# Kernel tuning notes

Hardware: AMD Instinct MI355X
Metric: run time of the kernel (lower is better)

The kernel has to match this reference:

```python
import jax, jax.numpy as jnp
import numpy as np

EMBED_DIM = 1024
NUM_HEADS = 16
HEAD_DIM = EMBED_DIM // NUM_HEADS


def setup_inputs() -> dict:
    key = jax.random.key(0)
    ks = jax.random.split(key, 5)
    B, N, E = 2, 2048, EMBED_DIM
    scale = E ** -0.5
    return {
        "x": jax.random.normal(ks[0], (B, N, E), dtype=jnp.float32),
        "w_qkv": jax.random.normal(ks[1], (E, 3 * E), dtype=jnp.float32) * scale,
        "b_qkv": jnp.zeros((3 * E,), dtype=jnp.float32),
        "w_proj": jax.random.normal(ks[2], (E, E), dtype=jnp.float32) * scale,
        "b_proj": jnp.zeros((E,), dtype=jnp.float32),
    }


def reference(x, w_qkv, b_qkv, w_proj, b_proj):
    B, N, E = x.shape
    H, D = NUM_HEADS, HEAD_DIM
    qkv = x @ w_qkv + b_qkv                      # [B,N,3E]
    qkv = qkv.reshape(B, N, 3, H, D)
    q = qkv[:, :, 0].transpose(0, 2, 1, 3)        # [B,H,N,D]
    k = qkv[:, :, 1].transpose(0, 2, 1, 3)
    v = qkv[:, :, 2].transpose(0, 2, 1, 3)
    attn = jnp.einsum('bhnd,bhmd->bhnm', q, k) * (D ** -0.5)
    attn = jax.nn.softmax(attn, axis=-1)          # dropout is identity in eval mode
    out = jnp.einsum('bhnm,bhmd->bhnd', attn, v)  # [B,H,N,D]
    out = out.transpose(0, 2, 1, 3).reshape(B, N, E)
    return out @ w_proj + b_proj
```

## Files before the change

kernel.cpp:

```cpp
#include <hip/hip_runtime.h>
#include <hip/hip_bf16.h>
#include <cstdint>
#include <cstddef>


typedef __attribute__((ext_vector_type(8))) short short8;
typedef __attribute__((ext_vector_type(4))) short short4v;
typedef __attribute__((ext_vector_type(4))) float f32x4;

#define MFMA16(a, b, c) __builtin_amdgcn_mfma_f32_16x16x32_bf16((a), (b), (c), 0, 0, 0)
#define EXP2F(x) __builtin_amdgcn_exp2f(x)

__device__ __forceinline__ float b2f(short s) {
  union { unsigned u; float f; } x; x.u = ((unsigned)(unsigned short)s) << 16; return x.f;
}
__device__ __forceinline__ short f2b(float f) {
  union { __hip_bfloat16 h; short s; } u; u.h = __float2bfloat16(f); return u.s;
}
__device__ __forceinline__ void async_lds16(const void* g, void* l) {
  __builtin_amdgcn_global_load_lds(
      (const __attribute__((address_space(1))) void*)g,
      (__attribute__((address_space(3))) void*)l, 16, 0, 0);
}

__global__ __launch_bounds__(256) void cast_f32_bf16(const float* __restrict__ in,
                                                     short* __restrict__ out, int n4) {
  for (int idx = blockIdx.x * 256 + threadIdx.x; idx < n4; idx += 1024 * 256) {
    f32x4 v = ((const f32x4*)in)[idx];
    short4v o;
    #pragma unroll
    for (int e = 0; e < 4; ++e) o[e] = f2b(v[e]);
    ((short4v*)out)[idx] = o;
  }
}

__global__ __launch_bounds__(256) void transpose_cast_w(const float* __restrict__ wqkv,
                                                        short* __restrict__ wqkvT,
                                                        const float* __restrict__ wproj,
                                                        short* __restrict__ wprojT) {
  __shared__ float tile[64][65];
  int b = blockIdx.x;
  const float* in;
  short* out;
  int C, bx, by;
  if (b < 768) { in = wqkv;  out = wqkvT;  C = 3072; bx = b % 48; by = b / 48; }
  else { b -= 768; in = wproj; out = wprojT; C = 1024; bx = b % 16; by = b / 16; }
  const int R = 1024;
  int c0 = bx * 64, r0 = by * 64;
  int tx = threadIdx.x & 63, ty = threadIdx.x >> 6;
  #pragma unroll
  for (int i = ty; i < 64; i += 4)
    tile[i][tx] = in[(size_t)(r0 + i) * C + c0 + tx];
  __syncthreads();
  #pragma unroll
  for (int i = ty; i < 64; i += 4)
    out[(size_t)(c0 + i) * R + r0 + tx] = f2b(tile[tx][i]);
}

__global__ __launch_bounds__(256, 3) void gemm_qkv(const short* __restrict__ xb,
                                                   const short* __restrict__ wT,
                                                   const float* __restrict__ bias,
                                                   short* __restrict__ Qb,
                                                   short* __restrict__ Kb,
                                                   short* __restrict__ Vt) {
  __shared__ short lds_a[128 * 64];
  __shared__ short lds_b[128 * 64];
  const int tid = threadIdx.x, wid = tid >> 6, lane = tid & 63;
  const int lg = lane >> 4, lr = lane & 15;
  const int lin = blockIdx.x;
  const int swz = (lin & 7) * 96 + (lin >> 3);
  const int m0 = (swz & 31) * 128, n0 = (swz >> 5) * 128;
  const int wr = wid >> 1, wc = wid & 1;
  const int K = 1024;
  const int sm = lr & 7;

  f32x4 acc[4][4];
  #pragma unroll
  for (int i = 0; i < 4; ++i)
    #pragma unroll
    for (int j = 0; j < 4; ++j) acc[i][j] = (f32x4)0.0f;

  for (int k0 = 0; k0 < K; k0 += 64) {
    #pragma unroll
    for (int it = 0; it < 4; ++it) {
      int chunk = it * 256 + tid;
      int row = chunk >> 3, kc = ((chunk & 7) ^ (row & 7)) * 8;
      async_lds16(xb + (size_t)(m0 + row) * K + k0 + kc, lds_a + chunk * 8);
      async_lds16(wT + (size_t)(n0 + row) * K + k0 + kc, lds_b + chunk * 8);
    }
    __syncthreads();
    #pragma unroll
    for (int kk = 0; kk < 2; ++kk) {
      short8 af[4], bfr[4];
      #pragma unroll
      for (int i = 0; i < 4; ++i)
        af[i] = *(const short8*)&lds_a[(wr * 64 + i * 16 + lr) * 64 +
                                       (((kk * 4 + lg) ^ sm) * 8)];
      #pragma unroll
      for (int j = 0; j < 4; ++j)
        bfr[j] = *(const short8*)&lds_b[(wc * 64 + j * 16 + lr) * 64 +
                                        (((kk * 4 + lg) ^ sm) * 8)];
      #pragma unroll
      for (int i = 0; i < 4; ++i)
        #pragma unroll
        for (int j = 0; j < 4; ++j) acc[i][j] = MFMA16(af[i], bfr[j], acc[i][j]);
    }
    __syncthreads();
  }

  #pragma unroll
  for (int i = 0; i < 4; ++i) {
    int gm = m0 + wr * 64 + i * 16 + lg * 4;
    int bb = gm >> 11, n = gm & 2047;
    #pragma unroll
    for (int j = 0; j < 4; ++j) {
      int gc = n0 + wc * 64 + j * 16 + lr;
      float bv = bias[gc];
      int which = gc >> 10;
      int h = (gc >> 6) & 15;
      int dd = gc & 63;
      size_t qkbase = ((size_t)((bb * 16 + h) * 2048 + n)) * 64 + dd;
      if (which == 2) {
        size_t vtbase = ((size_t)((bb * 16 + h) * 64 + dd)) * 2048 + n;
        short4v pv;
        #pragma unroll
        for (int r = 0; r < 4; ++r) pv[r] = f2b(acc[i][j][r] + bv);
        *(short4v*)&Vt[vtbase] = pv;
      } else {
        short* dst = (which == 0) ? Qb : Kb;
        #pragma unroll
        for (int r = 0; r < 4; ++r)
          dst[qkbase + (size_t)r * 64] = f2b(acc[i][j][r] + bv);
      }
    }
  }
}

__global__ __launch_bounds__(512) void attn_fwd(const short* __restrict__ Qb,
                                                const short* __restrict__ Kb,
                                                const short* __restrict__ Vt,
                                                short* __restrict__ aob) {
  __shared__ short k_lds[3][64 * 64];
  __shared__ short v_lds[3][64 * 64];
  __shared__ short p_lds[8 * 16 * 64];
  const int tid = threadIdx.x, wid = tid >> 6, lane = tid & 63;
  const int lg = lane >> 4, lr = lane & 15;
  const int lin = blockIdx.x;
  const int swz = (lin & 7) * 64 + (lin >> 3);
  const int qt = swz & 15, bh = swz >> 4;
  const int q0 = qt * 128 + wid * 16;
  const short* Qbh = Qb + (size_t)bh * 2048 * 64;
  const short* Kbh = Kb + (size_t)bh * 2048 * 64;
  const short* Vbh = Vt + (size_t)bh * 64 * 2048;
  const int rm = (lr >> 1) & 7;

  const int srow = tid >> 3;
  const int ssrc = ((tid & 7) ^ ((srow >> 1) & 7)) * 8;

  int pw[4], pr[2];
  #pragma unroll
  for (int jt = 0; jt < 4; ++jt)
    pw[jt] = wid * 1024 + lr * 64 + (((jt * 2 + (lg >> 1)) ^ rm) * 8) + (lg & 1) * 4;
  #pragma unroll
  for (int kk = 0; kk < 2; ++kk)
    pr[kk] = wid * 1024 + lr * 64 + (((kk * 4 + lg) ^ rm) * 8);

  short8 ones;
  #pragma unroll
  for (int e = 0; e < 8; ++e) ones[e] = (short)0x3F80;

  short8 qf[2];
  #pragma unroll
  for (int kk = 0; kk < 2; ++kk) {
    qf[kk] = *(const short8*)(Qbh + (size_t)(q0 + lr) * 64 + kk * 32 + lg * 8);
    #pragma unroll
    for (int e = 0; e < 8; ++e) qf[kk][e] = f2b(b2f(qf[kk][e]) * 0.1803368801f);
  }

  f32x4 o[4], o_l;
  #pragma unroll
  for (int dt = 0; dt < 4; ++dt) o[dt] = (f32x4)0.0f;
  o_l = (f32x4)0.0f;
  float m_ = -__builtin_inff();

  async_lds16(Kbh + (size_t)srow * 64 + ssrc, &k_lds[0][tid * 8]);
  async_lds16(Vbh + (size_t)srow * 2048 + 0 + ssrc, &v_lds[0][tid * 8]);
  async_lds16(Kbh + (size_t)(64 + srow) * 64 + ssrc, &k_lds[1][tid * 8]);
  async_lds16(Vbh + (size_t)srow * 2048 + 64 + ssrc, &v_lds[1][tid * 8]);
  asm volatile("s_waitcnt vmcnt(2)" ::: "memory");
  __syncthreads();

  int cur = 0, nx2 = 2;
  for (int t = 0; t < 32; ++t) {
    if (t + 2 < 32) {
      int kvn = (t + 2) * 64;
      async_lds16(Kbh + (size_t)(kvn + srow) * 64 + ssrc, &k_lds[nx2][tid * 8]);
      async_lds16(Vbh + (size_t)srow * 2048 + kvn + ssrc, &v_lds[nx2][tid * 8]);
    }

    f32x4 s[4];
    #pragma unroll
    for (int jt = 0; jt < 4; ++jt) s[jt] = (f32x4)0.0f;
    #pragma unroll
    for (int jt = 0; jt < 4; ++jt)
      #pragma unroll
      for (int kk = 0; kk < 2; ++kk) {
        short8 kf = *(const short8*)&k_lds[cur][(jt * 16 + lr) * 64 +
                                               (((kk * 4 + lg) ^ rm) * 8)];
        s[jt] = MFMA16(kf, qf[kk], s[jt]);
      }

    float mj[4];
    #pragma unroll
    for (int jt = 0; jt < 4; ++jt)
      mj[jt] = fmaxf(fmaxf(s[jt][0], s[jt][1]), fmaxf(s[jt][2], s[jt][3]));
    float pmax = fmaxf(fmaxf(mj[0], mj[1]), fmaxf(mj[2], mj[3]));
    pmax = fmaxf(pmax, __shfl_xor(pmax, 16));
    pmax = fmaxf(pmax, __shfl_xor(pmax, 32));
    if (!__all(pmax - m_ <= 8.0f)) {
      float mn = fmaxf(m_, pmax);
      float corr = EXP2F(m_ - mn);
      m_ = mn;
      #pragma unroll
      for (int dt = 0; dt < 4; ++dt)
        #pragma unroll
        for (int r = 0; r < 4; ++r) o[dt][r] *= corr;
      #pragma unroll
      for (int r = 0; r < 4; ++r) o_l[r] *= corr;
    }

    #pragma unroll
    for (int jt = 0; jt < 4; ++jt) {
      short4v pv;
      pv[0] = f2b(EXP2F(s[jt][0] - m_));
      pv[1] = f2b(EXP2F(s[jt][1] - m_));
      pv[2] = f2b(EXP2F(s[jt][2] - m_));
      pv[3] = f2b(EXP2F(s[jt][3] - m_));
      *(short4v*)&p_lds[pw[jt]] = pv;
    }

    #pragma unroll
    for (int kk = 0; kk < 2; ++kk) {
      short8 pa = *(const short8*)&p_lds[pr[kk]];
      o_l = MFMA16(ones, pa, o_l);
      #pragma unroll
      for (int dt = 0; dt < 4; ++dt) {
        short8 vb = *(const short8*)&v_lds[cur][(dt * 16 + lr) * 64 +
                                               (((kk * 4 + lg) ^ rm) * 8)];
        o[dt] = MFMA16(vb, pa, o[dt]);
      }
    }

    if (t < 31) {
      if (t < 30) asm volatile("s_waitcnt vmcnt(2)" ::: "memory");
      else        asm volatile("s_waitcnt vmcnt(0)" ::: "memory");
      __syncthreads();
    }
    cur = (cur == 2) ? 0 : cur + 1;
    nx2 = (nx2 == 2) ? 0 : nx2 + 1;
  }

  const int bb = bh >> 4, h = bh & 15;
  const float inv_l = __frcp_rn(o_l[0]);
  #pragma unroll
  for (int dt = 0; dt < 4; ++dt) {
    short4v ov;
    #pragma unroll
    for (int r = 0; r < 4; ++r) ov[r] = f2b(o[dt][r] * inv_l);
    *(short4v*)&aob[(size_t)(bb * 2048 + q0 + lr) * 1024 + h * 64 + dt * 16 + lg * 4] = ov;
  }
}

__global__ __launch_bounds__(256, 2) void gemm_proj(const short* __restrict__ aob,
                                                    const short* __restrict__ wT,
                                                    const float* __restrict__ bias,
                                                    float* __restrict__ out) {
  __shared__ short lds_a[64 * 64];
  __shared__ short lds_b[128 * 64];
  const int tid = threadIdx.x, wid = tid >> 6, lane = tid & 63;
  const int lg = lane >> 4, lr = lane & 15;
  const int lin = blockIdx.x;
  const int swz = (lin & 7) * 64 + (lin >> 3);
  const int m0 = (swz & 63) * 64, n0 = (swz >> 6) * 128;
  const int mw = wid >> 1, nw = wid & 1;
  const int K = 1024;
  const int sm = lr & 7;

  f32x4 acc[2][4];
  #pragma unroll
  for (int i = 0; i < 2; ++i)
    #pragma unroll
    for (int j = 0; j < 4; ++j) acc[i][j] = (f32x4)0.0f;

  for (int k0 = 0; k0 < K; k0 += 64) {
    #pragma unroll
    for (int it = 0; it < 2; ++it) {
      int chunk = it * 256 + tid;
      int row = chunk >> 3, kc = ((chunk & 7) ^ (row & 7)) * 8;
      async_lds16(aob + (size_t)(m0 + row) * K + k0 + kc, lds_a + chunk * 8);
    }
    #pragma unroll
    for (int it = 0; it < 4; ++it) {
      int chunk = it * 256 + tid;
      int row = chunk >> 3, kc = ((chunk & 7) ^ (row & 7)) * 8;
      async_lds16(wT + (size_t)(n0 + row) * K + k0 + kc, lds_b + chunk * 8);
    }
    __syncthreads();
    #pragma unroll
    for (int kk = 0; kk < 2; ++kk) {
      short8 af[2], bfr[4];
      #pragma unroll
      for (int i = 0; i < 2; ++i)
        af[i] = *(const short8*)&lds_a[(mw * 32 + i * 16 + lr) * 64 +
                                       (((kk * 4 + lg) ^ sm) * 8)];
      #pragma unroll
      for (int j = 0; j < 4; ++j)
        bfr[j] = *(const short8*)&lds_b[(nw * 64 + j * 16 + lr) * 64 +
                                        (((kk * 4 + lg) ^ sm) * 8)];
      #pragma unroll
      for (int i = 0; i < 2; ++i)
        #pragma unroll
        for (int j = 0; j < 4; ++j) acc[i][j] = MFMA16(af[i], bfr[j], acc[i][j]);
    }
    __syncthreads();
  }

  #pragma unroll
  for (int i = 0; i < 2; ++i) {
    int gm = m0 + mw * 32 + i * 16 + lg * 4;
    #pragma unroll
    for (int j = 0; j < 4; ++j) {
      int gc = n0 + nw * 64 + j * 16 + lr;
      float bv = bias[gc];
      #pragma unroll
      for (int r = 0; r < 4; ++r)
        out[(size_t)(gm + r) * 1024 + gc] = acc[i][j][r] + bv;
    }
  }
}

extern "C" void kernel_launch(void* const* d_in, const int* in_sizes, int n_in,
                              void* d_out, int out_size, void* d_ws, size_t ws_size,
                              hipStream_t stream) {
  const float* x     = (const float*)d_in[0];
  const float* wqkv  = (const float*)d_in[1];
  const float* bqkv  = (const float*)d_in[2];
  const float* wproj = (const float*)d_in[3];
  const float* bproj = (const float*)d_in[4];
  float* out = (float*)d_out;

  char* ws = (char*)d_ws;
  short* xb     = (short*)ws; ws += (size_t)4096 * 1024 * 2;
  short* wqkvT  = (short*)ws; ws += (size_t)3072 * 1024 * 2;
  short* wprojT = (short*)ws; ws += (size_t)1024 * 1024 * 2;
  short* Qb     = (short*)ws; ws += (size_t)32 * 2048 * 64 * 2;
  short* Kb     = (short*)ws; ws += (size_t)32 * 2048 * 64 * 2;
  short* Vt     = (short*)ws; ws += (size_t)32 * 64 * 2048 * 2;
  short* aob    = (short*)ws; ws += (size_t)4096 * 1024 * 2;

  cast_f32_bf16<<<1024, 256, 0, stream>>>(x, xb, 4096 * 1024 / 4);
  transpose_cast_w<<<1024, 256, 0, stream>>>(wqkv, wqkvT, wproj, wprojT);
  gemm_qkv<<<768, 256, 0, stream>>>(xb, wqkvT, bqkv, Qb, Kb, Vt);
  attn_fwd<<<512, 512, 0, stream>>>(Qb, Kb, Vt, aob);
  gemm_proj<<<512, 256, 0, stream>>>(aob, wprojT, bproj, out);
}
```

Baseline: 193.0 us.

## Process two KV tiles per attention iteration and merge preprocessing kernels

The attention loop now handles two 64-wide KV tiles per iteration with four LDS buffers in a double-pair ping-pong. This halves the barriers, the row-max reductions and the rescale checks per KV element. In exchange the prefetch now waits with vmcnt(0), so load latency is hidden only one iteration ahead, and LDS use grows. Separately, the x cast and the weight transpose/cast kernels are merged into one launch to cut launch overhead.

```diff
diff --git a/kernel.cpp b/kernel.cpp
--- a/kernel.cpp
+++ b/kernel.cpp
@@ -23,23 +23,25 @@
       (__attribute__((address_space(3))) void*)l, 16, 0, 0);
 }
 
-__global__ __launch_bounds__(256) void cast_f32_bf16(const float* __restrict__ in,
-                                                     short* __restrict__ out, int n4) {
-  for (int idx = blockIdx.x * 256 + threadIdx.x; idx < n4; idx += 1024 * 256) {
-    f32x4 v = ((const f32x4*)in)[idx];
-    short4v o;
-    #pragma unroll
-    for (int e = 0; e < 4; ++e) o[e] = f2b(v[e]);
-    ((short4v*)out)[idx] = o;
-  }
-}
-
-__global__ __launch_bounds__(256) void transpose_cast_w(const float* __restrict__ wqkv,
-                                                        short* __restrict__ wqkvT,
-                                                        const float* __restrict__ wproj,
-                                                        short* __restrict__ wprojT) {
+__global__ __launch_bounds__(256) void preproc(const float* __restrict__ wqkv,
+                                               short* __restrict__ wqkvT,
+                                               const float* __restrict__ wproj,
+                                               short* __restrict__ wprojT,
+                                               const float* __restrict__ x,
+                                               short* __restrict__ xb) {
+  int b = blockIdx.x;
+  if (b >= 1024) {
+    int n4 = 4096 * 1024 / 4;
+    for (int idx = (b - 1024) * 256 + threadIdx.x; idx < n4; idx += 512 * 256) {
+      f32x4 v = ((const f32x4*)x)[idx];
+      short4v o;
+      #pragma unroll
+      for (int e = 0; e < 4; ++e) o[e] = f2b(v[e]);
+      ((short4v*)xb)[idx] = o;
+    }
+    return;
+  }
   __shared__ float tile[64][65];
-  int b = blockIdx.x;
   const float* in;
   short* out;
   int C, bx, by;
@@ -140,8 +142,8 @@
                                                 const short* __restrict__ Kb,
                                                 const short* __restrict__ Vt,
                                                 short* __restrict__ aob) {
-  __shared__ short k_lds[3][64 * 64];
-  __shared__ short v_lds[3][64 * 64];
+  __shared__ short k_lds[4][64 * 64];
+  __shared__ short v_lds[4][64 * 64];
   __shared__ short p_lds[8 * 16 * 64];
   const int tid = threadIdx.x, wid = tid >> 6, lane = tid & 63;
   const int lg = lane >> 4, lr = lane & 15;
@@ -156,6 +158,9 @@
 
   const int srow = tid >> 3;
   const int ssrc = ((tid & 7) ^ ((srow >> 1) & 7)) * 8;
+  #define STAGE64(buf, kv0)                                                   \
+    async_lds16(Kbh + (size_t)((kv0) + srow) * 64 + ssrc, &k_lds[buf][tid * 8]); \
+    async_lds16(Vbh + (size_t)srow * 2048 + (kv0) + ssrc, &v_lds[buf][tid * 8]);
 
   int pw[4], pr[2];
   #pragma unroll
@@ -183,38 +188,42 @@
   o_l = (f32x4)0.0f;
   float m_ = -__builtin_inff();
 
-  async_lds16(Kbh + (size_t)srow * 64 + ssrc, &k_lds[0][tid * 8]);
-  async_lds16(Vbh + (size_t)srow * 2048 + 0 + ssrc, &v_lds[0][tid * 8]);
-  async_lds16(Kbh + (size_t)(64 + srow) * 64 + ssrc, &k_lds[1][tid * 8]);
-  async_lds16(Vbh + (size_t)srow * 2048 + 64 + ssrc, &v_lds[1][tid * 8]);
-  asm volatile("s_waitcnt vmcnt(2)" ::: "memory");
+  STAGE64(0, 0)
+  STAGE64(1, 64)
+  asm volatile("s_waitcnt vmcnt(0)" ::: "memory");
   __syncthreads();
 
-  int cur = 0, nx2 = 2;
-  for (int t = 0; t < 32; ++t) {
-    if (t + 2 < 32) {
-      int kvn = (t + 2) * 64;
-      async_lds16(Kbh + (size_t)(kvn + srow) * 64 + ssrc, &k_lds[nx2][tid * 8]);
-      async_lds16(Vbh + (size_t)srow * 2048 + kvn + ssrc, &v_lds[nx2][tid * 8]);
-    }
-
-    f32x4 s[4];
-    #pragma unroll
-    for (int jt = 0; jt < 4; ++jt) s[jt] = (f32x4)0.0f;
-    #pragma unroll
-    for (int jt = 0; jt < 4; ++jt)
-      #pragma unroll
-      for (int kk = 0; kk < 2; ++kk) {
-        short8 kf = *(const short8*)&k_lds[cur][(jt * 16 + lr) * 64 +
-                                               (((kk * 4 + lg) ^ rm) * 8)];
-        s[jt] = MFMA16(kf, qf[kk], s[jt]);
-      }
-
-    float mj[4];
-    #pragma unroll
-    for (int jt = 0; jt < 4; ++jt)
-      mj[jt] = fmaxf(fmaxf(s[jt][0], s[jt][1]), fmaxf(s[jt][2], s[jt][3]));
-    float pmax = fmaxf(fmaxf(mj[0], mj[1]), fmaxf(mj[2], mj[3]));
+  for (int tp = 0; tp < 16; ++tp) {
+    const int t0 = tp * 2;
+    const int b0 = (tp & 1) * 2, b1 = b0 + 1;
+    if (tp < 15) {
+      const int c0 = (b0 + 2) & 3, c1 = (b1 + 2) & 3;
+      STAGE64(c0, (t0 + 2) * 64)
+      STAGE64(c1, (t0 + 3) * 64)
+    }
+
+    f32x4 s[8];
+    #pragma unroll
+    for (int j = 0; j < 8; ++j) s[j] = (f32x4)0.0f;
+    #pragma unroll
+    for (int c = 0; c < 2; ++c) {
+      const short* kb = k_lds[c ? b1 : b0];
+      #pragma unroll
+      for (int jt = 0; jt < 4; ++jt)
+        #pragma unroll
+        for (int kk = 0; kk < 2; ++kk) {
+          short8 kf = *(const short8*)&kb[(jt * 16 + lr) * 64 +
+                                          (((kk * 4 + lg) ^ rm) * 8)];
+          s[c * 4 + jt] = MFMA16(kf, qf[kk], s[c * 4 + jt]);
+        }
+    }
+
+    float mj[8];
+    #pragma unroll
+    for (int j = 0; j < 8; ++j)
+      mj[j] = fmaxf(fmaxf(s[j][0], s[j][1]), fmaxf(s[j][2], s[j][3]));
+    float pmax = fmaxf(fmaxf(fmaxf(mj[0], mj[1]), fmaxf(mj[2], mj[3])),
+                       fmaxf(fmaxf(mj[4], mj[5]), fmaxf(mj[6], mj[7])));
     pmax = fmaxf(pmax, __shfl_xor(pmax, 16));
     pmax = fmaxf(pmax, __shfl_xor(pmax, 32));
     if (!__all(pmax - m_ <= 8.0f)) {
@@ -230,35 +239,37 @@
     }
 
     #pragma unroll
-    for (int jt = 0; jt < 4; ++jt) {
-      short4v pv;
-      pv[0] = f2b(EXP2F(s[jt][0] - m_));
-      pv[1] = f2b(EXP2F(s[jt][1] - m_));
-      pv[2] = f2b(EXP2F(s[jt][2] - m_));
-      pv[3] = f2b(EXP2F(s[jt][3] - m_));
-      *(short4v*)&p_lds[pw[jt]] = pv;
-    }
-
-    #pragma unroll
-    for (int kk = 0; kk < 2; ++kk) {
-      short8 pa = *(const short8*)&p_lds[pr[kk]];
-      o_l = MFMA16(ones, pa, o_l);
-      #pragma unroll
-      for (int dt = 0; dt < 4; ++dt) {
-        short8 vb = *(const short8*)&v_lds[cur][(dt * 16 + lr) * 64 +
-                                               (((kk * 4 + lg) ^ rm) * 8)];
-        o[dt] = MFMA16(vb, pa, o[dt]);
+    for (int c = 0; c < 2; ++c) {
+      #pragma unroll
+      for (int jt = 0; jt < 4; ++jt) {
+        f32x4 sv = s[c * 4 + jt];
+        short4v pv;
+        pv[0] = f2b(EXP2F(sv[0] - m_));
+        pv[1] = f2b(EXP2F(sv[1] - m_));
+        pv[2] = f2b(EXP2F(sv[2] - m_));
+        pv[3] = f2b(EXP2F(sv[3] - m_));
+        *(short4v*)&p_lds[pw[jt]] = pv;
       }
-    }
-
-    if (t < 31) {
-      if (t < 30) asm volatile("s_waitcnt vmcnt(2)" ::: "memory");
-      else        asm volatile("s_waitcnt vmcnt(0)" ::: "memory");
+      const short* vb0 = v_lds[c ? b1 : b0];
+      #pragma unroll
+      for (int kk = 0; kk < 2; ++kk) {
+        short8 pa = *(const short8*)&p_lds[pr[kk]];
+        o_l = MFMA16(ones, pa, o_l);
+        #pragma unroll
+        for (int dt = 0; dt < 4; ++dt) {
+          short8 vb = *(const short8*)&vb0[(dt * 16 + lr) * 64 +
+                                           (((kk * 4 + lg) ^ rm) * 8)];
+          o[dt] = MFMA16(vb, pa, o[dt]);
+        }
+      }
+    }
+
+    if (tp < 15) {
+      asm volatile("s_waitcnt vmcnt(0)" ::: "memory");
       __syncthreads();
     }
-    cur = (cur == 2) ? 0 : cur + 1;
-    nx2 = (nx2 == 2) ? 0 : nx2 + 1;
-  }
+  }
+  #undef STAGE64
 
   const int bb = bh >> 4, h = bh & 15;
   const float inv_l = __frcp_rn(o_l[0]);
@@ -358,8 +369,7 @@
   short* Vt     = (short*)ws; ws += (size_t)32 * 64 * 2048 * 2;
   short* aob    = (short*)ws; ws += (size_t)4096 * 1024 * 2;
 
-  cast_f32_bf16<<<1024, 256, 0, stream>>>(x, xb, 4096 * 1024 / 4);
-  transpose_cast_w<<<1024, 256, 0, stream>>>(wqkv, wqkvT, wproj, wprojT);
+  preproc<<<1536, 256, 0, stream>>>(wqkv, wqkvT, wproj, wprojT, x, xb);
   gemm_qkv<<<768, 256, 0, stream>>>(xb, wqkvT, bqkv, Qb, Kb, Vt);
   attn_fwd<<<512, 512, 0, stream>>>(Qb, Kb, Vt, aob);
   gemm_proj<<<512, 256, 0, stream>>>(aob, wprojT, bproj, out);
```

Result: faster. 183.1 us (-5.2%).
